# Kernel optimization log

Measured on AMD Instinct MI355X. Metric: run time of the kernel, lower is better.

Reference implementation:

```python
import jax, jax.numpy as jnp
import numpy as np

D_MODEL = 1024
N_HEADS = 16
D_FF = 4096
EPS = 1e-5


def setup_inputs() -> dict:
    key = jax.random.key(0)
    ks = jax.random.split(key, 16)
    s = 0.02
    d, f = D_MODEL, D_FF
    return {
        "x": jax.random.normal(ks[0], (4, 2048, d), dtype=jnp.float32),
        "WQ": jax.random.normal(ks[1], (d, d), dtype=jnp.float32) * s,
        "bQ": jnp.zeros((d,), dtype=jnp.float32),
        "WK": jax.random.normal(ks[2], (d, d), dtype=jnp.float32) * s,
        "bK": jnp.zeros((d,), dtype=jnp.float32),
        "WV": jax.random.normal(ks[3], (d, d), dtype=jnp.float32) * s,
        "bV": jnp.zeros((d,), dtype=jnp.float32),
        "WO": jax.random.normal(ks[4], (d, d), dtype=jnp.float32) * s,
        "bO": jnp.zeros((d,), dtype=jnp.float32),
        "W1": jax.random.normal(ks[5], (f, d), dtype=jnp.float32) * s,
        "b1": jnp.zeros((f,), dtype=jnp.float32),
        "W2": jax.random.normal(ks[6], (d, f), dtype=jnp.float32) * s,
        "b2": jnp.zeros((d,), dtype=jnp.float32),
        "g1": jnp.ones((d,), dtype=jnp.float32),
        "be1": jnp.zeros((d,), dtype=jnp.float32),
        "g2": jnp.ones((d,), dtype=jnp.float32),
        "be2": jnp.zeros((d,), dtype=jnp.float32),
    }


def _layernorm(x, g, b):
    mu = jnp.mean(x, axis=-1, keepdims=True)
    var = jnp.mean(jnp.square(x - mu), axis=-1, keepdims=True)
    return (x - mu) * jax.lax.rsqrt(var + EPS) * g + b


def reference(x, WQ, bQ, WK, bK, WV, bV, WO, bO, W1, b1, W2, b2, g1, be1, g2, be2):
    B, T, D = x.shape
    H, dk = N_HEADS, D // N_HEADS
    # projections (torch Linear: x @ W.T + b), reshape to [B,H,T,dk]
    q = (x @ WQ.T + bQ).reshape(B, T, H, dk).transpose(0, 2, 1, 3)
    k = (x @ WK.T + bK).reshape(B, T, H, dk).transpose(0, 2, 1, 3)
    v = (x @ WV.T + bV).reshape(B, T, H, dk).transpose(0, 2, 1, 3)
    scores = jnp.einsum("bhqd,bhkd->bhqk", q, k) / jnp.sqrt(jnp.float32(dk))
    causal = jnp.tril(jnp.ones((T, T), dtype=bool))
    scores = jnp.where(causal[None, None], scores, jnp.float32(-jnp.inf))
    attn = jax.nn.softmax(scores, axis=-1)
    out = jnp.einsum("bhqk,bhkd->bhqd", attn, v)
    out = out.transpose(0, 2, 1, 3).reshape(B, T, D)
    attn_out = out @ WO.T + bO
    x = _layernorm(x + attn_out, g1, be1)
    ff = jax.nn.relu(x @ W1.T + b1) @ W2.T + b2
    return _layernorm(x + ff, g2, be2)
```

## Files before the change

### kernel.cpp

```cpp
#include <hip/hip_runtime.h>

typedef unsigned short u16;
typedef unsigned int u32;
typedef __bf16 bf16x8 __attribute__((ext_vector_type(8)));
typedef float f32x4 __attribute__((ext_vector_type(4)));
typedef float f32x16 __attribute__((ext_vector_type(16)));

__device__ __forceinline__ u16 f2bf(float f) {
  u32 u = __builtin_bit_cast(u32, f);
  u = (u + 0x7fffu + ((u >> 16) & 1u)) >> 16;
  return (u16)u;
}
__device__ __forceinline__ float bf2f(u16 h) {
  return __builtin_bit_cast(float, ((u32)h) << 16);
}

__device__ __forceinline__ void gll16(const u16* g, u16* l) {
  __builtin_amdgcn_global_load_lds((const __attribute__((address_space(1))) void*)g,
                                   (__attribute__((address_space(3))) void*)l, 16, 0, 0);
}

__device__ __forceinline__ void barrier() {
  asm volatile("" ::: "memory");
  __builtin_amdgcn_s_barrier();
  asm volatile("" ::: "memory");
}
__device__ __forceinline__ void waitv8() { asm volatile("s_waitcnt vmcnt(8)" ::: "memory"); }
__device__ __forceinline__ void waitv4() { asm volatile("s_waitcnt vmcnt(4)" ::: "memory"); }
__device__ __forceinline__ void waitv0() { asm volatile("s_waitcnt vmcnt(0)" ::: "memory"); }

__global__ __launch_bounds__(256) void cvt_all(const float* __restrict__ x,
                                               const float* __restrict__ WQ,
                                               const float* __restrict__ WK,
                                               const float* __restrict__ WV,
                                               const float* __restrict__ WO,
                                               const float* __restrict__ W1,
                                               const float* __restrict__ W2,
                                               u16* __restrict__ xb,
                                               u16* __restrict__ wqkvb,
                                               u16* __restrict__ wob,
                                               u16* __restrict__ w1b,
                                               u16* __restrict__ w2b) {
  const int S = 1 << 20;
  int i = (blockIdx.x * 256 + threadIdx.x) * 4;
  const float* src;
  u16* dst;
  if (i < 8 * S) { src = x + i; dst = xb + i; }
  else {
    int j = i - 8 * S;
    if (j < 3 * S)      { src = (j < S) ? WQ + j : (j < 2 * S) ? WK + (j - S) : WV + (j - 2 * S);
                          dst = wqkvb + j; }
    else if (j < 4 * S) { src = WO + (j - 3 * S); dst = wob + (j - 3 * S); }
    else if (j < 8 * S) { src = W1 + (j - 4 * S); dst = w1b + (j - 4 * S); }
    else                { src = W2 + (j - 8 * S); dst = w2b + (j - 8 * S); }
  }
  float4 v = *(const float4*)src;
  uint2 o;
  o.x = (u32)f2bf(v.x) | ((u32)f2bf(v.y) << 16);
  o.y = (u32)f2bf(v.z) | ((u32)f2bf(v.w) << 16);
  *(uint2*)dst = o;
}

template <int RELU, int QKV, int SPLIT>
__global__ __launch_bounds__(512, 2) void gemm256(const u16* __restrict__ A,
                                                  const u16* __restrict__ W,
                                                  const float* __restrict__ bias0,
                                                  void* __restrict__ C0,
                                                  int M, int N, int K,
                                                  const float* __restrict__ bias1,
                                                  void* __restrict__ C1,
                                                  const float* __restrict__ bias2,
                                                  void* __restrict__ C2,
                                                  int NBN) {
  __shared__ alignas(16) u16 lds[4 * 16384];
  const int tid = threadIdx.x;
  const int id = blockIdx.x;
  const int xcd = id & 7, r = id >> 3;
  int bm, bn, kz = 0, koff = 0, KL = K;
  if (SPLIT) {
    bn = (r & 3) << 8;
    const int q = r >> 2;
    bm = ((q & 3) * 8 + xcd) << 8;
    kz = q >> 2;
    KL = K >> 1;
    koff = kz * KL;
  } else {
    bn = (r % NBN) << 8;
    bm = ((r / NBN) * 8 + xcd) << 8;
  }
  const int wave = tid >> 6, lane = tid & 63;
  const int lr = lane & 15, quad = lane >> 4;
  const int wm = (wave >> 2) << 7;
  const int wn = (wave & 3) << 6;

  const int lrow = lane >> 2;
  const int lch = (lane & 3) ^ ((lane >> 3) & 3);
  const u16* Asrc = A + (size_t)(bm + wave * 16 + lrow) * K + koff + lch * 8;
  const u16* Wsrc = W + (size_t)(bn + wave * 16 + lrow) * K + koff + lch * 8;
  const size_t half = (size_t)128 * K;
  u16* dstbase = lds + wave * 512;

  const int NT = KL >> 5;
  const int fro = (quad ^ ((lr >> 1) & 3)) * 8;
  f32x4 acc[8][4] = {};

  #pragma unroll
  for (int t = 0; t < 3; t++) {
    u16* d = dstbase + t * 16384;
    gll16(Asrc + (size_t)t * 32, d);
    gll16(Asrc + (size_t)t * 32 + half, d + 4096);
    gll16(Wsrc + (size_t)t * 32, d + 8192);
    gll16(Wsrc + (size_t)t * 32 + half, d + 12288);
  }
  waitv8();
  barrier();

  for (int t = 0; t < NT; t++) {
    const u16* sa = lds + (t & 3) * 16384;
    const u16* sb = sa + 8192;
    const int tp = (t + 3 < NT) ? t + 3 : NT - 1;
    u16* d = dstbase + ((t + 3) & 3) * 16384;
    const size_t ko = (size_t)tp * 32;

    bf16x8 af[4], bfr[4];
    #pragma unroll
    for (int mi = 0; mi < 4; mi++)
      af[mi] = *(const bf16x8*)(sa + (wm + mi * 16 + lr) * 32 + fro);
    #pragma unroll
    for (int ni = 0; ni < 4; ni++)
      bfr[ni] = *(const bf16x8*)(sb + (wn + ni * 16 + lr) * 32 + fro);
    gll16(Asrc + ko, d);
    gll16(Asrc + ko + half, d + 4096);
    barrier();
    asm volatile("s_waitcnt lgkmcnt(0)" ::: "memory");
    __builtin_amdgcn_s_setprio(1);
    #pragma unroll
    for (int mi = 0; mi < 4; mi++)
      #pragma unroll
      for (int ni = 0; ni < 4; ni++)
        acc[mi][ni] = __builtin_amdgcn_mfma_f32_16x16x32_bf16(af[mi], bfr[ni], acc[mi][ni], 0, 0, 0);
    __builtin_amdgcn_s_setprio(0);
    barrier();

    #pragma unroll
    for (int mi = 0; mi < 4; mi++)
      af[mi] = *(const bf16x8*)(sa + (wm + 64 + mi * 16 + lr) * 32 + fro);
    gll16(Wsrc + ko, d + 8192);
    gll16(Wsrc + ko + half, d + 12288);
    barrier();
    asm volatile("s_waitcnt lgkmcnt(0)" ::: "memory");
    __builtin_amdgcn_s_setprio(1);
    #pragma unroll
    for (int mi = 0; mi < 4; mi++)
      #pragma unroll
      for (int ni = 0; ni < 4; ni++)
        acc[4 + mi][ni] = __builtin_amdgcn_mfma_f32_16x16x32_bf16(af[mi], bfr[ni], acc[4 + mi][ni], 0, 0, 0);
    __builtin_amdgcn_s_setprio(0);
    waitv8();
    barrier();
  }
  waitv0();

  const float* bp = bias0;
  void* outp = C0;
  float scale = 1.0f;
  int cb = bn, Nout = N, seg = 0;
  if (QKV) {
    Nout = 1024;
    seg = bn >> 10;
    cb = bn & 1023;
    if (seg == 0) scale = 0.125f * 1.44269504089f;
    else if (seg == 1) { bp = bias1; outp = C1; }
    else { bp = bias2; outp = C2; }
  }
  if (SPLIT && kz) outp = C1;

  if (QKV && seg == 2) {
    #pragma unroll
    for (int ni = 0; ni < 4; ni++) {
      const int col = cb + wn + ni * 16 + lr;
      const int hh = col >> 6, dl = col & 63;
      const float bv = bp[col];
      #pragma unroll
      for (int mi = 0; mi < 8; mi++) {
        const int row0 = bm + wm + mi * 16 + quad * 4;
        const int bb = row0 >> 11, tt = row0 & 2047;
        u16 pk[4];
        #pragma unroll
        for (int rg = 0; rg < 4; rg++) pk[rg] = f2bf(acc[mi][ni][rg] + bv);
        uint2 val;
        val.x = (u32)pk[0] | ((u32)pk[1] << 16);
        val.y = (u32)pk[2] | ((u32)pk[3] << 16);
        *(uint2*)(((u16*)outp) + ((size_t)((bb * 16 + hh) * 64 + dl)) * 2048 + tt) = val;
      }
    }
    return;
  }

  #pragma unroll
  for (int ni = 0; ni < 4; ni++) {
    const int col = cb + wn + ni * 16 + lr;
    const float bv = (SPLIT && kz) ? 0.0f : bp[col];
    #pragma unroll
    for (int mi = 0; mi < 8; mi++) {
      #pragma unroll
      for (int rg = 0; rg < 4; rg++) {
        int row = bm + wm + mi * 16 + quad * 4 + rg;
        float v = (acc[mi][ni][rg] + bv) * scale;
        if (RELU) v = fmaxf(v, 0.0f);
        ((u16*)outp)[(size_t)row * Nout + col] = f2bf(v);
      }
    }
  }
}

__global__ __launch_bounds__(256) void attn_mfma(const u16* __restrict__ qb,
                                                 const u16* __restrict__ kb,
                                                 const u16* __restrict__ vt,
                                                 u16* __restrict__ ctxb, int T) {
  __shared__ alignas(16) u16 sK[2][64 * 64];
  __shared__ alignas(16) u16 sVt[2][64 * 64];
  const int tid = threadIdx.x;
  const int i = blockIdx.x;
  const int g = (i & 7) | (((i >> 7) & 7) << 3);
  const int p = (i >> 3) & 15;
  const int h = g >> 2, b = g & 3;
  const size_t base = ((size_t)(b * T)) * 1024 + h * 64;
  const size_t vbase = ((size_t)((b * 16 + h) * 64)) * T;
  const int lane = tid & 63, wave = tid >> 6;
  const int l31 = lane & 31, hh = lane >> 5;

  const int srow = lane >> 3;
  const int sch = ((lane & 7) ^ srow) * 8;

  const int qtA = 31 - p, qtB = p;
  const int vw = (wave + (i & 3)) & 3;
  const int myqt = (vw >> 1) ? qtB : qtA;
  const int q0w = myqt * 64 + (vw & 1) * 32;

#define STAGEKV(ktt, slot) {                                                       \
    const int kc_ = ((ktt) <= qtA) ? (ktt) : qtA;                                  \
    _Pragma("unroll") for (int j_ = 0; j_ < 2; j_++) {                             \
      const int rb_ = (wave * 2 + j_) * 8;                                         \
      const int rr_ = rb_ + srow;                                                  \
      gll16(kb + base + (size_t)(kc_ * 64 + rr_) * 1024 + sch, sK[slot] + rb_ * 64);\
      gll16(vt + vbase + (size_t)rr_ * T + (size_t)(kc_ * 64) + sch, sVt[slot] + rb_ * 64);\
    } }

  bf16x8 qf[4];
  #pragma unroll
  for (int ds = 0; ds < 4; ds++) {
    uint4 uq = *(const uint4*)(qb + base + (size_t)(q0w + l31) * 1024 + ds * 16 + hh * 8);
    qf[ds] = __builtin_bit_cast(bf16x8, uq);
  }
  f32x16 o0 = {}, o1 = {};
  float rsum = 0.0f;
  const int fs8 = (l31 & 7);

  STAGEKV(0, 0);

  for (int kt = 0; kt <= qtA; kt++) {
    barrier();
    STAGEKV(kt + 1, (kt + 1) & 1);
    waitv4();
    barrier();
    if (kt <= myqt) {
      const u16* sKc = sK[kt & 1];
      const u16* sVc = sVt[kt & 1];

      f32x16 s0v = {}, s1v = {};
      #pragma unroll
      for (int ds = 0; ds < 4; ds++) {
        const int co = ((2 * ds + hh) ^ fs8) * 8;
        bf16x8 kf0 = *(const bf16x8*)(sKc + l31 * 64 + co);
        bf16x8 kf1 = *(const bf16x8*)(sKc + (32 + l31) * 64 + co);
        s0v = __builtin_amdgcn_mfma_f32_32x32x16_bf16(kf0, qf[ds], s0v, 0, 0, 0);
        s1v = __builtin_amdgcn_mfma_f32_32x32x16_bf16(kf1, qf[ds], s1v, 0, 0, 0);
      }

      if (kt == myqt) {
        const int qloc = ((vw & 1) << 5) + l31;
        #pragma unroll
        for (int rg = 0; rg < 16; rg++) {
          const int key = (rg & 3) + 8 * (rg >> 2) + 4 * hh;
          if (key > qloc) s0v[rg] = -1e30f;
          if (key + 32 > qloc) s1v[rg] = -1e30f;
        }
      }

      float e[32];
      #pragma unroll
      for (int rg = 0; rg < 16; rg++) {
        e[rg] = __builtin_amdgcn_exp2f(s0v[rg]);
        e[16 + rg] = __builtin_amdgcn_exp2f(s1v[rg]);
        rsum += e[rg] + e[16 + rg];
      }

      union PW { u32 w[4]; bf16x8 v; } pf[4];
      #pragma unroll
      for (int t = 0; t < 2; t++) {
        #pragma unroll
        for (int sl = 0; sl < 2; sl++) {
          const int rb = t * 16 + sl * 8;
          u32 wa = __builtin_amdgcn_perm(__builtin_bit_cast(u32, e[rb + 1]), __builtin_bit_cast(u32, e[rb + 0]), 0x07060302u);
          u32 wb = __builtin_amdgcn_perm(__builtin_bit_cast(u32, e[rb + 5]), __builtin_bit_cast(u32, e[rb + 4]), 0x07060302u);
          u32 wc = __builtin_amdgcn_perm(__builtin_bit_cast(u32, e[rb + 3]), __builtin_bit_cast(u32, e[rb + 2]), 0x07060302u);
          u32 wd = __builtin_amdgcn_perm(__builtin_bit_cast(u32, e[rb + 7]), __builtin_bit_cast(u32, e[rb + 6]), 0x07060302u);
          asm("v_permlane32_swap_b32 %0, %1" : "+v"(wa), "+v"(wb));
          asm("v_permlane32_swap_b32 %0, %1" : "+v"(wc), "+v"(wd));
          pf[t * 2 + sl].w[0] = wa; pf[t * 2 + sl].w[1] = wc;
          pf[t * 2 + sl].w[2] = wb; pf[t * 2 + sl].w[3] = wd;
        }
      }

      #pragma unroll
      for (int s = 0; s < 4; s++) {
        const int co = ((2 * s + hh) ^ fs8) * 8;
        bf16x8 vf0 = *(const bf16x8*)(sVc + l31 * 64 + co);
        bf16x8 vf1 = *(const bf16x8*)(sVc + (32 + l31) * 64 + co);
        o0 = __builtin_amdgcn_mfma_f32_32x32x16_bf16(pf[s].v, vf0, o0, 0, 0, 0);
        o1 = __builtin_amdgcn_mfma_f32_32x32x16_bf16(pf[s].v, vf1, o1, 0, 0, 0);
      }
    }
  }
  waitv0();
#undef STAGEKV

  rsum += __shfl_xor(rsum, 32);
  float inv = 1.0f / rsum;
  #pragma unroll
  for (int rg = 0; rg < 16; rg++) {
    const int qr = (rg & 3) + 8 * (rg >> 2) + 4 * hh;
    float iv = __shfl(inv, qr);
    const size_t rowoff = base + (size_t)(q0w + qr) * 1024;
    ctxb[rowoff + l31] = f2bf(o0[rg] * iv);
    ctxb[rowoff + 32 + l31] = f2bf(o1[rg] * iv);
  }
}

template <int ABF>
__global__ __launch_bounds__(256) void ln_kernel(const void* __restrict__ a,
                                                 const u16* __restrict__ b,
                                                 const u16* __restrict__ c,
                                                 const float* __restrict__ g,
                                                 const float* __restrict__ be,
                                                 float* __restrict__ of32,
                                                 u16* __restrict__ obf) {
  const int row = blockIdx.x;
  const int tid = threadIdx.x;
  const size_t base = (size_t)row * 1024;
  const int cc = tid * 4;
  float a0, a1, a2, a3;
  if (ABF) {
    uint2 ua = *(const uint2*)((const u16*)a + base + cc);
    a0 = bf2f(ua.x & 0xffff); a1 = bf2f(ua.x >> 16);
    a2 = bf2f(ua.y & 0xffff); a3 = bf2f(ua.y >> 16);
  } else {
    float4 xa = *(const float4*)((const float*)a + base + cc);
    a0 = xa.x; a1 = xa.y; a2 = xa.z; a3 = xa.w;
  }
  uint2 ub = *(const uint2*)(b + base + cc);
  uint2 uc = *(const uint2*)(c + base + cc);
  float v0 = a0 + bf2f(ub.x & 0xffff) + bf2f(uc.x & 0xffff);
  float v1 = a1 + bf2f(ub.x >> 16)    + bf2f(uc.x >> 16);
  float v2 = a2 + bf2f(ub.y & 0xffff) + bf2f(uc.y & 0xffff);
  float v3 = a3 + bf2f(ub.y >> 16)    + bf2f(uc.y >> 16);
  float s1 = v0 + v1 + v2 + v3;
  float s2 = v0 * v0 + v1 * v1 + v2 * v2 + v3 * v3;
  for (int off = 1; off < 64; off <<= 1) {
    s1 += __shfl_xor(s1, off);
    s2 += __shfl_xor(s2, off);
  }
  __shared__ float red[8];
  int wv = tid >> 6;
  if ((tid & 63) == 0) { red[wv] = s1; red[4 + wv] = s2; }
  __syncthreads();
  s1 = red[0] + red[1] + red[2] + red[3];
  s2 = red[4] + red[5] + red[6] + red[7];
  float mu = s1 * (1.0f / 1024.0f);
  float var = s2 * (1.0f / 1024.0f) - mu * mu;
  float rs = rsqrtf(var + 1e-5f);
  float4 gv = *(const float4*)(g + cc);
  float4 bev = *(const float4*)(be + cc);
  float y0 = (v0 - mu) * rs * gv.x + bev.x;
  float y1 = (v1 - mu) * rs * gv.y + bev.y;
  float y2 = (v2 - mu) * rs * gv.z + bev.z;
  float y3 = (v3 - mu) * rs * gv.w + bev.w;
  if (of32) {
    float4 o = make_float4(y0, y1, y2, y3);
    *(float4*)(of32 + base + cc) = o;
  }
  if (obf) {
    uint2 o;
    o.x = (u32)f2bf(y0) | ((u32)f2bf(y1) << 16);
    o.y = (u32)f2bf(y2) | ((u32)f2bf(y3) << 16);
    *(uint2*)(obf + base + cc) = o;
  }
}

extern "C" void kernel_launch(void* const* d_in, const int* in_sizes, int n_in,
                              void* d_out, int out_size, void* d_ws, size_t ws_size,
                              hipStream_t stream) {
  const int Mtok = 8192, D = 1024, F = 4096, T = 2048;
  const float* x   = (const float*)d_in[0];
  const float* WQ  = (const float*)d_in[1];
  const float* bQ  = (const float*)d_in[2];
  const float* WK  = (const float*)d_in[3];
  const float* bK  = (const float*)d_in[4];
  const float* WV  = (const float*)d_in[5];
  const float* bV  = (const float*)d_in[6];
  const float* WO  = (const float*)d_in[7];
  const float* bO  = (const float*)d_in[8];
  const float* W1  = (const float*)d_in[9];
  const float* b1  = (const float*)d_in[10];
  const float* W2  = (const float*)d_in[11];
  const float* b2  = (const float*)d_in[12];
  const float* g1  = (const float*)d_in[13];
  const float* be1 = (const float*)d_in[14];
  const float* g2  = (const float*)d_in[15];
  const float* be2 = (const float*)d_in[16];

  char* ws = (char*)d_ws;
  const size_t MB = 1024 * 1024;
  u16*  xb     = (u16*)(ws + 0);
  u16*  wqkvb  = (u16*)(ws + 16 * MB);
  u16*  wob    = (u16*)(ws + 22 * MB);
  u16*  w1b    = (u16*)(ws + 24 * MB);
  u16*  w2b    = (u16*)(ws + 32 * MB);
  u16*  qb     = (u16*)(ws + 40 * MB);
  u16*  kb     = (u16*)(ws + 56 * MB);
  u16*  vtb    = (u16*)(ws + 72 * MB);
  u16*  ctxb   = (u16*)(ws + 88 * MB);
  u16*  wp0    = (u16*)(ws + 104 * MB);
  u16*  wp1    = (u16*)(ws + 120 * MB);
  u16*  h1b    = (u16*)(ws + 136 * MB);
  u16*  ff1b   = (u16*)(ws + 40 * MB);
  u16*  fp0    = (u16*)(ws + 0);
  u16*  fp1    = (u16*)(ws + 16 * MB);
  float* out   = (float*)d_out;

  dim3 blk(256);
  dim3 blk512(512);
  cvt_all<<<(20 << 20) / 1024, blk, 0, stream>>>(x, WQ, WK, WV, WO, W1, W2,
                                                 xb, wqkvb, wob, w1b, w2b);

  gemm256<0, 1, 0><<<dim3(384), blk512, 0, stream>>>(xb, wqkvb, bQ, qb, Mtok, 3072, D,
                                                     bK, kb, bV, vtb, 12);
  attn_mfma<<<dim3(1024), blk, 0, stream>>>(qb, kb, vtb, ctxb, T);

  gemm256<0, 0, 1><<<dim3(256), blk512, 0, stream>>>(ctxb, wob, bO, wp0, Mtok, D, D,
                                                     nullptr, wp1, nullptr, nullptr, 4);
  ln_kernel<0><<<Mtok, blk, 0, stream>>>(x, wp0, wp1, g1, be1, nullptr, h1b);

  gemm256<1, 0, 0><<<dim3(512), blk512, 0, stream>>>(h1b, w1b, b1, ff1b, Mtok, F, D,
                                                     nullptr, nullptr, nullptr, nullptr, 16);
  gemm256<0, 0, 1><<<dim3(256), blk512, 0, stream>>>(ff1b, w2b, b2, fp0, Mtok, D, F,
                                                     nullptr, fp1, nullptr, nullptr, 4);
  ln_kernel<1><<<Mtok, blk, 0, stream>>>(h1b, fp0, fp1, g2, be2, out, (u16*)nullptr);
}
```

Measured before the change: 503.9 us.

## Split attention KV range across wave pairs with LDS reduction, one q-tile per block

Each attention block now handles a single 64-row query tile, and its four waves split into two pairs that process even and odd key tiles in parallel. Partial outputs and row sums are combined through LDS at the end. The grid doubles to 2048 blocks, ordered so the longest causal tiles launch first. The change drops the paired short/long q-tile load balancing and the double-buffered prefetch, and each iteration now waits for all loads with vmcnt(0), which exposes load latency.

```diff
diff --git a/kernel.cpp b/kernel.cpp
--- a/kernel.cpp
+++ b/kernel.cpp
@@ -26,7 +26,6 @@
   asm volatile("" ::: "memory");
 }
 __device__ __forceinline__ void waitv8() { asm volatile("s_waitcnt vmcnt(8)" ::: "memory"); }
-__device__ __forceinline__ void waitv4() { asm volatile("s_waitcnt vmcnt(4)" ::: "memory"); }
 __device__ __forceinline__ void waitv0() { asm volatile("s_waitcnt vmcnt(0)" ::: "memory"); }
 
 __global__ __launch_bounds__(256) void cvt_all(const float* __restrict__ x,
@@ -218,34 +217,22 @@
                                                  const u16* __restrict__ kb,
                                                  const u16* __restrict__ vt,
                                                  u16* __restrict__ ctxb, int T) {
-  __shared__ alignas(16) u16 sK[2][64 * 64];
-  __shared__ alignas(16) u16 sVt[2][64 * 64];
+  __shared__ alignas(16) u16 shm[4 * 4096];
   const int tid = threadIdx.x;
   const int i = blockIdx.x;
-  const int g = (i & 7) | (((i >> 7) & 7) << 3);
-  const int p = (i >> 3) & 15;
+  const int g = i & 63;
+  const int p = 31 - (i >> 6);
   const int h = g >> 2, b = g & 3;
   const size_t base = ((size_t)(b * T)) * 1024 + h * 64;
   const size_t vbase = ((size_t)((b * 16 + h) * 64)) * T;
   const int lane = tid & 63, wave = tid >> 6;
   const int l31 = lane & 31, hh = lane >> 5;
-
+  const int sub = wave & 1;
+  const int kh = wave >> 1;
   const int srow = lane >> 3;
   const int sch = ((lane & 7) ^ srow) * 8;
-
-  const int qtA = 31 - p, qtB = p;
-  const int vw = (wave + (i & 3)) & 3;
-  const int myqt = (vw >> 1) ? qtB : qtA;
-  const int q0w = myqt * 64 + (vw & 1) * 32;
-
-#define STAGEKV(ktt, slot) {                                                       \
-    const int kc_ = ((ktt) <= qtA) ? (ktt) : qtA;                                  \
-    _Pragma("unroll") for (int j_ = 0; j_ < 2; j_++) {                             \
-      const int rb_ = (wave * 2 + j_) * 8;                                         \
-      const int rr_ = rb_ + srow;                                                  \
-      gll16(kb + base + (size_t)(kc_ * 64 + rr_) * 1024 + sch, sK[slot] + rb_ * 64);\
-      gll16(vt + vbase + (size_t)rr_ * T + (size_t)(kc_ * 64) + sch, sVt[slot] + rb_ * 64);\
-    } }
+  const int fs8 = l31 & 7;
+  const int q0w = p * 64 + sub * 32;
 
   bf16x8 qf[4];
   #pragma unroll
@@ -255,18 +242,27 @@
   }
   f32x16 o0 = {}, o1 = {};
   float rsum = 0.0f;
-  const int fs8 = (l31 & 7);
-
-  STAGEKV(0, 0);
-
-  for (int kt = 0; kt <= qtA; kt++) {
-    barrier();
-    STAGEKV(kt + 1, (kt + 1) & 1);
-    waitv4();
-    barrier();
-    if (kt <= myqt) {
-      const u16* sKc = sK[kt & 1];
-      const u16* sVc = sVt[kt & 1];
+
+  const int NI = (p >> 1) + 1;
+  for (int j = 0; j < NI; j++) {
+    const int ke = 2 * j;
+    const int ko = (2 * j + 1 <= p) ? 2 * j + 1 : p;
+    barrier();
+    #pragma unroll
+    for (int jj = 0; jj < 2; jj++) {
+      const int rb = wave * 16 + jj * 8;
+      const int rr = rb + srow;
+      gll16(kb + base + (size_t)(ke * 64 + rr) * 1024 + sch, shm + rb * 64);
+      gll16(kb + base + (size_t)(ko * 64 + rr) * 1024 + sch, shm + 4096 + rb * 64);
+      gll16(vt + vbase + (size_t)rr * T + (size_t)(ke * 64) + sch, shm + 8192 + rb * 64);
+      gll16(vt + vbase + (size_t)rr * T + (size_t)(ko * 64) + sch, shm + 12288 + rb * 64);
+    }
+    waitv0();
+    barrier();
+    const int kt = 2 * j + kh;
+    if (kt <= p) {
+      const u16* sKc = shm + kh * 4096;
+      const u16* sVc = shm + 8192 + kh * 4096;
 
       f32x16 s0v = {}, s1v = {};
       #pragma unroll
@@ -278,8 +274,8 @@
         s1v = __builtin_amdgcn_mfma_f32_32x32x16_bf16(kf1, qf[ds], s1v, 0, 0, 0);
       }
 
-      if (kt == myqt) {
-        const int qloc = ((vw & 1) << 5) + l31;
+      if (kt == p) {
+        const int qloc = (sub << 5) + l31;
         #pragma unroll
         for (int rg = 0; rg < 16; rg++) {
           const int key = (rg & 3) + 8 * (rg >> 2) + 4 * hh;
@@ -323,18 +319,35 @@
       }
     }
   }
-  waitv0();
-#undef STAGEKV
 
   rsum += __shfl_xor(rsum, 32);
-  float inv = 1.0f / rsum;
-  #pragma unroll
-  for (int rg = 0; rg < 16; rg++) {
-    const int qr = (rg & 3) + 8 * (rg >> 2) + 4 * hh;
-    float iv = __shfl(inv, qr);
-    const size_t rowoff = base + (size_t)(q0w + qr) * 1024;
-    ctxb[rowoff + l31] = f2bf(o0[rg] * iv);
-    ctxb[rowoff + 32 + l31] = f2bf(o1[rg] * iv);
+  barrier();
+  float* red = (float*)shm;
+  if (kh == 1) {
+    #pragma unroll
+    for (int rg = 0; rg < 16; rg++) {
+      red[sub * 2112 + rg * 64 + lane] = o0[rg];
+      red[sub * 2112 + (16 + rg) * 64 + lane] = o1[rg];
+    }
+    red[sub * 2112 + 2048 + lane] = rsum;
+  }
+  barrier();
+  if (kh == 0) {
+    #pragma unroll
+    for (int rg = 0; rg < 16; rg++) {
+      o0[rg] += red[sub * 2112 + rg * 64 + lane];
+      o1[rg] += red[sub * 2112 + (16 + rg) * 64 + lane];
+    }
+    rsum += red[sub * 2112 + 2048 + lane];
+    float inv = 1.0f / rsum;
+    #pragma unroll
+    for (int rg = 0; rg < 16; rg++) {
+      const int qr = (rg & 3) + 8 * (rg >> 2) + 4 * hh;
+      float iv = __shfl(inv, qr);
+      const size_t rowoff = base + (size_t)(q0w + qr) * 1024;
+      ctxb[rowoff + l31] = f2bf(o0[rg] * iv);
+      ctxb[rowoff + 32 + l31] = f2bf(o1[rg] * iv);
+    }
   }
 }
 
@@ -446,7 +459,7 @@
 
   gemm256<0, 1, 0><<<dim3(384), blk512, 0, stream>>>(xb, wqkvb, bQ, qb, Mtok, 3072, D,
                                                      bK, kb, bV, vtb, 12);
-  attn_mfma<<<dim3(1024), blk, 0, stream>>>(qb, kb, vtb, ctxb, T);
+  attn_mfma<<<dim3(2048), blk, 0, stream>>>(qb, kb, vtb, ctxb, T);
 
   gemm256<0, 0, 1><<<dim3(256), blk512, 0, stream>>>(ctxb, wob, bO, wp0, Mtok, D, D,
                                                      nullptr, wp1, nullptr, nullptr, 4);
```

New measurement: 489.0 us. -3.0%, faster.
